# Optimization experiments

Measured on AMD Instinct MI355X. Metric: run time of the kernel, lower is better.

The kernel has to match this reference:

```python
import jax, jax.numpy as jnp
import numpy as np

B, N, NF, DEG = 128, 1024, 64, 16
NH = 128          # top-level n_hidden
H = NH // 2       # per-branch hidden (64)
NNODES = B * N
NEDGES = NNODES * DEG
ANG = 2


def _lin(key, fi, fo):
    k1, k2 = jax.random.split(key)
    s = 1.0 / np.sqrt(fi)
    return (jax.random.uniform(k1, (fi, fo), minval=-s, maxval=s, dtype=jnp.float32),
            jax.random.uniform(k2, (fo,), minval=-s, maxval=s, dtype=jnp.float32))

_PARAM_DEFS = [("W_pre1_a", "b_pre1_a", NF, H), ("W_pre2_a", "b_pre2_a", H, H), ("W_gcn_a", "b_gcn_a", H, H),
               ("W_pre1_b", "b_pre1_b", NF, H), ("W_pre2_b", "b_pre2_b", H, H), ("W_gcn_b", "b_gcn_b", H, H),
               ("W_lin1", "b_lin1", 2 * NH + 1, NH), ("W_lin2", "b_lin2", NH, NH // 2),
               ("W_lin3", "b_lin3", NH // 2, 1), ("W_cb", "b_cb", NH // 2, 1),
               ("W_om", "b_om", NH // 2, ANG), ("W_th", "b_th", NH // 2, ANG), ("W_ph", "b_ph", NH // 2, ANG)]


def setup_inputs() -> dict:
    key = jax.random.key(0)
    ks = jax.random.split(key, 24)

    def edges(k):
        # block-structured edges: each graph g owns nodes [g*N, (g+1)*N)
        e = jax.random.randint(k, (2, NEDGES), 0, N, dtype=jnp.int32)
        off = (jnp.arange(NEDGES, dtype=jnp.int32) // (N * DEG)) * N
        return e + off[None, :]

    batch = jnp.arange(NNODES, dtype=jnp.int32) // N
    inp = {
        "x_a": jax.random.normal(ks[0], (NNODES, NF), dtype=jnp.float32),
        "edge_index_a": edges(ks[1]),
        "edge_attr_a": jax.random.uniform(ks[2], (NEDGES,), dtype=jnp.float32),
        "x_a_batch": batch,
        "x_b": jax.random.normal(ks[3], (NNODES, NF), dtype=jnp.float32),
        "edge_index_b": edges(ks[4]),
        "edge_attr_b": jax.random.uniform(ks[5], (NEDGES,), dtype=jnp.float32),
        "x_b_batch": batch,
        "linker_size": jax.random.uniform(ks[6], (B, 1), dtype=jnp.float32),
    }
    for i, (wn, bn, fi, fo) in enumerate(_PARAM_DEFS):
        w, b = _lin(ks[7 + i], fi, fo)
        inp[wn] = w
        inp[bn] = b
    return inp


def _gcn(x, W, b, src, dst, ew, n):
    # GCNConv with edge weights and self loops (fill_value=1):
    #   out = D^{-1/2} (A + I) D^{-1/2} (x W) + b
    h = x @ W
    deg = jax.ops.segment_sum(ew, dst, num_segments=n) + 1.0
    dinv = jax.lax.rsqrt(deg)
    norm = dinv[src] * ew * dinv[dst]                        # [E]
    out = jax.ops.segment_sum(h[src] * norm[:, None], dst, num_segments=n)
    out = out + h * (dinv * dinv)[:, None]                   # self-loop contribution
    return out + b


def _branch(x, ei, ea, bat, Wp1, bp1, Wp2, bp2, Wg, bg):
    x = jax.nn.relu(x @ Wp1 + bp1)
    x = jax.nn.relu(x @ Wp2 + bp2)
    x = jax.nn.relu(_gcn(x, Wg, bg, ei[0], ei[1], ea, x.shape[0]))
    s = jax.ops.segment_sum(x, bat, num_segments=B)          # gsp: global sum pool
    cnt = jax.ops.segment_sum(jnp.ones((x.shape[0], 1), x.dtype), bat, num_segments=B)
    return jnp.concatenate([s, s / cnt], axis=1)             # [B, 2H] = [gsp || gap(mean)]


def reference(x_a, edge_index_a, edge_attr_a, x_a_batch,
              x_b, edge_index_b, edge_attr_b, x_b_batch, linker_size,
              W_pre1_a, b_pre1_a, W_pre2_a, b_pre2_a, W_gcn_a, b_gcn_a,
              W_pre1_b, b_pre1_b, W_pre2_b, b_pre2_b, W_gcn_b, b_gcn_b,
              W_lin1, b_lin1, W_lin2, b_lin2, W_lin3, b_lin3,
              W_cb, b_cb, W_om, b_om, W_th, b_th, W_ph, b_ph):
    xa = _branch(x_a, edge_index_a, edge_attr_a, x_a_batch,
                 W_pre1_a, b_pre1_a, W_pre2_a, b_pre2_a, W_gcn_a, b_gcn_a)
    xb = _branch(x_b, edge_index_b, edge_attr_b, x_b_batch,
                 W_pre1_b, b_pre1_b, W_pre2_b, b_pre2_b, W_gcn_b, b_gcn_b)
    x = jnp.concatenate([xa, xb, linker_size], axis=1)       # [B, 2*NH+1]
    x = jax.nn.relu(x @ W_lin1 + b_lin1)                     # dropout p=0.0 -> identity
    x = jax.nn.relu(x @ W_lin2 + b_lin2)
    ca = x @ W_lin3 + b_lin3                                 # loss_type='bce' -> no sigmoid
    cb = x @ W_cb + b_cb
    om = x @ W_om + b_om
    th = x @ W_th + b_th
    ph = x @ W_ph + b_ph
    return (ca, cb, om, th, ph)
```

## Files before the change

kernel.cpp:

```cpp
#include <hip/hip_runtime.h>
#include <hip/hip_bf16.h>

#define NNODES 131072
#define NEDGES 2097152
#define NB     128
#define NPG    1024
#define EPG    16384

#define OFF_DEG      0
#define OFF_POOLED   (OFF_DEG + 2*NNODES)
#define OFF_WT       (OFF_POOLED + 2*NB*64)
#define OFF_H        (OFF_WT + 6*4096)
#define OFF_CNT      (OFF_H + (size_t)2*NNODES*64)
#define OFF_ROWSTART (OFF_CNT + 2*NNODES)
#define OFF_CURSOR   (OFF_ROWSTART + 2*NNODES)
#define OFF_CSR      (OFF_CURSOR + 2*NNODES)
#define WS_NEEDED    ((OFF_CSR + (size_t)4*NEDGES) * 4)

#define CSRB_LDS 145408

typedef __attribute__((ext_vector_type(8))) short bfrag;
typedef __attribute__((ext_vector_type(4))) float f32x4;

__device__ __forceinline__ unsigned short f2bf(float v) {
    unsigned int u = __float_as_uint(v);
    unsigned int r = (u + 0x7fffu + ((u >> 16) & 1u)) >> 16;
    return (unsigned short)r;
}
__device__ __forceinline__ float bf2f(unsigned short s) {
    return __uint_as_float(((unsigned int)s) << 16);
}

__global__ void wprep(const float* __restrict__ w0, const float* __restrict__ w1,
                      const float* __restrict__ w2, const float* __restrict__ w3,
                      const float* __restrict__ w4, const float* __restrict__ w5,
                      unsigned short* __restrict__ wf) {
    int m = blockIdx.x;
    const float* w = (m == 0) ? w0 : (m == 1) ? w1 : (m == 2) ? w2
                   : (m == 3) ? w3 : (m == 4) ? w4 : w5;
    for (int idx = threadIdx.x; idx < 4096; idx += blockDim.x) {
        int ft   = idx >> 10;
        int kt   = (idx >> 9) & 1;
        int lane = (idx >> 3) & 63;
        int i    = idx & 7;
        int f = ft * 16 + (lane & 15);
        int k = kt * 32 + ((lane >> 4) << 3) + i;
        float v = w[k * 64 + f];
        unsigned short hi = f2bf(v);
        unsigned short lo = f2bf(v - bf2f(hi));
        wf[m * 8192 + idx]        = hi;
        wf[m * 8192 + 4096 + idx] = lo;
    }
}

__global__ __launch_bounds__(512) void csr_build2(
    const int* __restrict__ eia, const float* __restrict__ eaa,
    const int* __restrict__ eib, const float* __restrict__ eab,
    float* __restrict__ deg, int* __restrict__ rowstart,
    int* __restrict__ cnt, float2* __restrict__ csr) {
    extern __shared__ char smem[];
    float2* scsr = (float2*)smem;
    float*  sdeg = (float*)(smem + 131072);
    int*    scnt = (int*)(smem + 135168);
    int*    scur = (int*)(smem + 139264);
    int*    sm   = (int*)(smem + 143360);
    const int g  = blockIdx.x;
    const int br = blockIdx.y;
    const int* ei   = br ? eib : eia;
    const float* ea = br ? eab : eaa;
    const int t     = threadIdx.x;
    const int ebase = g * EPG;
    const int nbase = g * NPG;

    for (int i = t; i < NPG; i += 512) { sdeg[i] = 0.f; scnt[i] = 0; }
    __syncthreads();

#pragma unroll 4
    for (int it = 0; it < EPG / 512; ++it) {
        int e = ebase + it * 512 + t;
        int d = ei[NEDGES + e] - nbase;
        float w = ea[e];
        atomicAdd(&scnt[d], 1);
        atomicAdd(&sdeg[d], w);
    }
    __syncthreads();

    for (int i = t; i < NPG; i += 512) {
        float dv = sdeg[i];
        deg[br * NNODES + nbase + i] = dv;
        sdeg[i] = rsqrtf(dv + 1.f);
    }

    int c0 = scnt[t * 2 + 0], c1 = scnt[t * 2 + 1];
    int T = c0 + c1;
    sm[t] = T;
    __syncthreads();
    for (int off = 1; off < 512; off <<= 1) {
        int v = (t >= off) ? sm[t - off] : 0;
        __syncthreads();
        sm[t] += v;
        __syncthreads();
    }
    int excl = sm[t] - T;
    int r0 = excl, r1 = excl + c0;
    int nout = br * NNODES + nbase + t * 2;
    rowstart[nout + 0] = ebase + r0;
    rowstart[nout + 1] = ebase + r1;
    cnt[nout + 0] = c0; cnt[nout + 1] = c1;
    scur[t * 2 + 0] = r0; scur[t * 2 + 1] = r1;
    __syncthreads();

#pragma unroll 4
    for (int it = 0; it < EPG / 512; ++it) {
        int e = ebase + it * 512 + t;
        int srcg = ei[e];
        int s = srcg - nbase;
        int d = ei[NEDGES + e] - nbase;
        float w = ea[e];
        int pos = atomicAdd(&scur[d], 1);
        float2 pr;
        pr.x = __int_as_float(srcg);
        pr.y = sdeg[s] * w * sdeg[d];
        scsr[pos] = pr;
    }
    __syncthreads();

    float4* dst4 = (float4*)(csr + (size_t)br * NEDGES + ebase);
    const float4* src4 = (const float4*)scsr;
    for (int i = t; i < 8192; i += 512) dst4[i] = src4[i];
}

__global__ __launch_bounds__(256) void csr_build(
    const int* __restrict__ eia, const float* __restrict__ eaa,
    const int* __restrict__ eib, const float* __restrict__ eab,
    float* __restrict__ deg, int* __restrict__ rowstart,
    int* __restrict__ cnt, float2* __restrict__ csr) {
    __shared__ float sdeg[NPG];
    __shared__ int   scnt[NPG];
    __shared__ int   scur[NPG];
    __shared__ int   sm[256];
    const int g  = blockIdx.x;
    const int br = blockIdx.y;
    const int* ei   = br ? eib : eia;
    const float* ea = br ? eab : eaa;
    const int t     = threadIdx.x;
    const int ebase = g * EPG;
    const int nbase = g * NPG;

    for (int i = t; i < NPG; i += 256) { sdeg[i] = 0.f; scnt[i] = 0; }
    __syncthreads();
#pragma unroll 4
    for (int it = 0; it < EPG / 256; ++it) {
        int e = ebase + it * 256 + t;
        int d = ei[NEDGES + e] - nbase;
        float w = ea[e];
        atomicAdd(&scnt[d], 1);
        atomicAdd(&sdeg[d], w);
    }
    __syncthreads();
    for (int i = t; i < NPG; i += 256) {
        float dv = sdeg[i];
        deg[br * NNODES + nbase + i] = dv;
        sdeg[i] = rsqrtf(dv + 1.f);
    }
    int c0 = scnt[t * 4 + 0], c1 = scnt[t * 4 + 1], c2 = scnt[t * 4 + 2], c3 = scnt[t * 4 + 3];
    int T = c0 + c1 + c2 + c3;
    sm[t] = T;
    __syncthreads();
    for (int off = 1; off < 256; off <<= 1) {
        int v = (t >= off) ? sm[t - off] : 0;
        __syncthreads();
        sm[t] += v;
        __syncthreads();
    }
    int excl = sm[t] - T;
    int base = ebase + excl;
    int r0 = base, r1 = base + c0, r2 = r1 + c1, r3 = r2 + c2;
    int nout = br * NNODES + nbase + t * 4;
    rowstart[nout + 0] = r0; rowstart[nout + 1] = r1;
    rowstart[nout + 2] = r2; rowstart[nout + 3] = r3;
    cnt[nout + 0] = c0; cnt[nout + 1] = c1; cnt[nout + 2] = c2; cnt[nout + 3] = c3;
    scur[t * 4 + 0] = r0; scur[t * 4 + 1] = r1;
    scur[t * 4 + 2] = r2; scur[t * 4 + 3] = r3;
    __syncthreads();
    float2* cso = csr + (size_t)br * NEDGES;
#pragma unroll 4
    for (int it = 0; it < EPG / 256; ++it) {
        int e = ebase + it * 256 + t;
        int srcg = ei[e];
        int s = srcg - nbase;
        int d = ei[NEDGES + e] - nbase;
        float w = ea[e];
        int pos = atomicAdd(&scur[d], 1);
        float2 pr;
        pr.x = __int_as_float(srcg);
        pr.y = sdeg[s] * w * sdeg[d];
        cso[pos] = pr;
    }
}

__global__ __launch_bounds__(256) void node_mlp_mfma(
    const float* __restrict__ xa, const float* __restrict__ xb,
    const unsigned short* __restrict__ wf,
    const float* __restrict__ b1a, const float* __restrict__ b2a,
    const float* __restrict__ b1b, const float* __restrict__ b2b,
    float* __restrict__ hout) {
    __shared__ float lds[4 * 16 * 65];
    const int br = blockIdx.y;
    const float* x = br ? xb : xa;
    const unsigned short* wfb = wf + br * 3 * 8192;
    const float* b1 = br ? b1b : b1a;
    const float* b2 = br ? b2b : b2a;
    const int wave = threadIdx.x >> 6;
    const int lane = threadIdx.x & 63;
    const int row  = lane & 15;
    const int kg   = lane >> 4;
    const int n0   = blockIdx.x * 64 + wave * 16;
    float* wlds = &lds[wave * 16 * 65];

    bfrag ahi[2], alo[2];
#pragma unroll
    for (int kt = 0; kt < 2; ++kt) {
        const float4* p = reinterpret_cast<const float4*>(
            x + (size_t)(n0 + row) * 64 + kt * 32 + kg * 8);
        float4 v0 = p[0], v1 = p[1];
        float vv[8] = {v0.x, v0.y, v0.z, v0.w, v1.x, v1.y, v1.z, v1.w};
        bfrag h, l;
#pragma unroll
        for (int i = 0; i < 8; ++i) {
            unsigned short hb = f2bf(vv[i]);
            unsigned short lb = f2bf(vv[i] - bf2f(hb));
            h[i] = (short)hb;
            l[i] = (short)lb;
        }
        ahi[kt] = h; alo[kt] = l;
    }

#pragma unroll
    for (int layer = 0; layer < 3; ++layer) {
        const unsigned short* wl = wfb + layer * 8192;
        bfrag bhi[4][2], blo[4][2];
#pragma unroll
        for (int ft = 0; ft < 4; ++ft)
#pragma unroll
            for (int kt = 0; kt < 2; ++kt) {
                bhi[ft][kt] = *reinterpret_cast<const bfrag*>(wl + ft * 1024 + kt * 512 + lane * 8);
                blo[ft][kt] = *reinterpret_cast<const bfrag*>(wl + 4096 + ft * 1024 + kt * 512 + lane * 8);
            }
        f32x4 acc[4];
#pragma unroll
        for (int ft = 0; ft < 4; ++ft) {
            float bv = (layer == 0) ? b1[ft * 16 + row]
                     : (layer == 1) ? b2[ft * 16 + row] : 0.f;
            acc[ft] = (f32x4){bv, bv, bv, bv};
        }
#pragma unroll
        for (int ft = 0; ft < 4; ++ft)
#pragma unroll
            for (int kt = 0; kt < 2; ++kt) {
                acc[ft] = __builtin_amdgcn_mfma_f32_16x16x32_bf16(ahi[kt], bhi[ft][kt], acc[ft], 0, 0, 0);
                acc[ft] = __builtin_amdgcn_mfma_f32_16x16x32_bf16(alo[kt], bhi[ft][kt], acc[ft], 0, 0, 0);
                acc[ft] = __builtin_amdgcn_mfma_f32_16x16x32_bf16(ahi[kt], blo[ft][kt], acc[ft], 0, 0, 0);
            }

        if (layer < 2) {
#pragma unroll
            for (int ft = 0; ft < 4; ++ft)
#pragma unroll
                for (int r = 0; r < 4; ++r)
                    wlds[(kg * 4 + r) * 65 + ft * 16 + row] = fmaxf(acc[ft][r], 0.f);
            __syncthreads();
#pragma unroll
            for (int kt = 0; kt < 2; ++kt) {
                const float* rp = &wlds[row * 65 + kt * 32 + kg * 8];
                bfrag h, l;
#pragma unroll
                for (int i = 0; i < 8; ++i) {
                    float v = rp[i];
                    unsigned short hb = f2bf(v);
                    unsigned short lb = f2bf(v - bf2f(hb));
                    h[i] = (short)hb;
                    l[i] = (short)lb;
                }
                ahi[kt] = h; alo[kt] = l;
            }
            __syncthreads();
        } else {
            float* hp = hout + (size_t)br * NNODES * 64 + (size_t)n0 * 64;
#pragma unroll
            for (int ft = 0; ft < 4; ++ft)
#pragma unroll
                for (int r = 0; r < 4; ++r)
                    hp[(kg * 4 + r) * 64 + ft * 16 + row] = acc[ft][r];
        }
    }
}

__global__ __launch_bounds__(256) void gcn_gather_pool(
    const int* __restrict__ rowstart, const int* __restrict__ cnt,
    const float2* __restrict__ csr, const float* __restrict__ deg,
    const float* __restrict__ h,
    const float* __restrict__ bga, const float* __restrict__ bgb,
    float* __restrict__ pooled) {
    __shared__ float red[256];
    const int bid  = blockIdx.x;
    const int xcd  = bid & 7;
    const int sub  = bid >> 3;
    const int gb   = xcd * 32 + (sub >> 4);
    const int blk  = sub & 15;
    const int br   = gb >> 7;
    const int g    = gb & 127;
    const int wave = threadIdx.x >> 6;
    const int lane = threadIdx.x & 63;
    const int n0   = g * NPG + blk * 64 + wave * 16;

    const int*    rs = rowstart + br * NNODES;
    const int*    ct = cnt + br * NNODES;
    const float2* cs = csr + (size_t)br * NEDGES;
    const float*  dg = deg + br * NNODES;
    const float*  hh = h + (size_t)br * NNODES * 64;
    const float bias = (br ? bgb : bga)[lane];

    float psum = 0.f;
    for (int j = 0; j < 16; ++j) {
        int n = n0 + j;
        int r = __builtin_amdgcn_readfirstlane(rs[n]);
        int c = __builtin_amdgcn_readfirstlane(ct[n]);
        float a0 = 0.f, a1 = 0.f, a2 = 0.f, a3 = 0.f;
        int i = 0;
        for (; i + 4 <= c; i += 4) {
            float2 p0 = cs[r + i + 0];
            float2 p1 = cs[r + i + 1];
            float2 p2 = cs[r + i + 2];
            float2 p3 = cs[r + i + 3];
            a0 = fmaf(p0.y, hh[(size_t)__float_as_int(p0.x) * 64 + lane], a0);
            a1 = fmaf(p1.y, hh[(size_t)__float_as_int(p1.x) * 64 + lane], a1);
            a2 = fmaf(p2.y, hh[(size_t)__float_as_int(p2.x) * 64 + lane], a2);
            a3 = fmaf(p3.y, hh[(size_t)__float_as_int(p3.x) * 64 + lane], a3);
        }
        for (; i < c; ++i) {
            float2 p = cs[r + i];
            a0 = fmaf(p.y, hh[(size_t)__float_as_int(p.x) * 64 + lane], a0);
        }
        float d = dg[n] + 1.f;
        float v = (a0 + a1) + (a2 + a3) + hh[(size_t)n * 64 + lane] * (1.f / d) + bias;
        psum += fmaxf(v, 0.f);
    }
    red[threadIdx.x] = psum;
    __syncthreads();
    if (wave == 0) {
        float s = red[lane] + red[64 + lane] + red[128 + lane] + red[192 + lane];
        unsafeAtomicAdd(&pooled[br * (NB * 64) + g * 64 + lane], s);
    }
}

__global__ __launch_bounds__(128) void final_mlp(
    const float* __restrict__ pooled, const float* __restrict__ linker,
    const float* __restrict__ W1, const float* __restrict__ b1,
    const float* __restrict__ W2, const float* __restrict__ b2,
    const float* __restrict__ W3, const float* __restrict__ b3,
    const float* __restrict__ Wcb, const float* __restrict__ bcb,
    const float* __restrict__ Wom, const float* __restrict__ bom,
    const float* __restrict__ Wth, const float* __restrict__ bth,
    const float* __restrict__ Wph, const float* __restrict__ bph,
    float* __restrict__ out) {
    __shared__ float inv[260];
    __shared__ float x1[128];
    __shared__ float x2[64];
    const int g = blockIdx.x;
    const int t = threadIdx.x;
    if (t < 64) {
        float pa = pooled[g * 64 + t];
        float pb = pooled[NB * 64 + g * 64 + t];
        inv[t]       = pa;
        inv[64 + t]  = pa * (1.f / 1024.f);
        inv[128 + t] = pb;
        inv[192 + t] = pb * (1.f / 1024.f);
    }
    if (t == 0) inv[256] = linker[g];
    __syncthreads();

    {
        float a = b1[t];
        for (int i = 0; i < 257; ++i) a = fmaf(inv[i], W1[i * 128 + t], a);
        x1[t] = fmaxf(a, 0.f);
    }
    __syncthreads();
    if (t < 64) {
        float a = b2[t];
        for (int i = 0; i < 128; ++i) a = fmaf(x1[i], W2[i * 64 + t], a);
        x2[t] = fmaxf(a, 0.f);
    }
    __syncthreads();
    if (t < 8) {
        if (t == 0) {
            float a = b3[0];
            for (int i = 0; i < 64; ++i) a = fmaf(x2[i], W3[i], a);
            out[g] = a;
        } else if (t == 1) {
            float a = bcb[0];
            for (int i = 0; i < 64; ++i) a = fmaf(x2[i], Wcb[i], a);
            out[128 + g] = a;
        } else if (t < 4) {
            int j = t - 2; float a = bom[j];
            for (int i = 0; i < 64; ++i) a = fmaf(x2[i], Wom[i * 2 + j], a);
            out[256 + g * 2 + j] = a;
        } else if (t < 6) {
            int j = t - 4; float a = bth[j];
            for (int i = 0; i < 64; ++i) a = fmaf(x2[i], Wth[i * 2 + j], a);
            out[512 + g * 2 + j] = a;
        } else {
            int j = t - 6; float a = bph[j];
            for (int i = 0; i < 64; ++i) a = fmaf(x2[i], Wph[i * 2 + j], a);
            out[768 + g * 2 + j] = a;
        }
    }
}

extern "C" void kernel_launch(void* const* d_in, const int* in_sizes, int n_in,
                              void* d_out, int out_size, void* d_ws, size_t ws_size,
                              hipStream_t stream) {
    const float* x_a  = (const float*)d_in[0];
    const int*   ei_a = (const int*)d_in[1];
    const float* ea_a = (const float*)d_in[2];
    const float* x_b  = (const float*)d_in[4];
    const int*   ei_b = (const int*)d_in[5];
    const float* ea_b = (const float*)d_in[6];
    const float* linker = (const float*)d_in[8];
    const float* W_pre1_a = (const float*)d_in[9];
    const float* b_pre1_a = (const float*)d_in[10];
    const float* W_pre2_a = (const float*)d_in[11];
    const float* b_pre2_a = (const float*)d_in[12];
    const float* W_gcn_a  = (const float*)d_in[13];
    const float* b_gcn_a  = (const float*)d_in[14];
    const float* W_pre1_b = (const float*)d_in[15];
    const float* b_pre1_b = (const float*)d_in[16];
    const float* W_pre2_b = (const float*)d_in[17];
    const float* b_pre2_b = (const float*)d_in[18];
    const float* W_gcn_b  = (const float*)d_in[19];
    const float* b_gcn_b  = (const float*)d_in[20];
    const float* W_lin1 = (const float*)d_in[21];
    const float* b_lin1 = (const float*)d_in[22];
    const float* W_lin2 = (const float*)d_in[23];
    const float* b_lin2 = (const float*)d_in[24];
    const float* W_lin3 = (const float*)d_in[25];
    const float* b_lin3 = (const float*)d_in[26];
    const float* W_cb = (const float*)d_in[27];
    const float* b_cb = (const float*)d_in[28];
    const float* W_om = (const float*)d_in[29];
    const float* b_om = (const float*)d_in[30];
    const float* W_th = (const float*)d_in[31];
    const float* b_th = (const float*)d_in[32];
    const float* W_ph = (const float*)d_in[33];
    const float* b_ph = (const float*)d_in[34];

    float* ws     = (float*)d_ws;
    float* deg    = ws + OFF_DEG;
    float* pooled = ws + OFF_POOLED;
    float* wtw    = ws + OFF_WT;
    float* h      = ws + OFF_H;
    int*   cnt      = (int*)(ws + OFF_CNT);
    int*   rowstart = (int*)(ws + OFF_ROWSTART);
    float2* csr     = (float2*)(ws + OFF_CSR);

    hipMemsetAsync(pooled, 0, 2 * NB * 64 * sizeof(float), stream);
    wprep<<<6, 256, 0, stream>>>(W_pre1_a, W_pre2_a, W_gcn_a,
                                 W_pre1_b, W_pre2_b, W_gcn_b,
                                 (unsigned short*)wtw);

    hipError_t attr_ok = hipFuncSetAttribute(
        reinterpret_cast<const void*>(&csr_build2),
        hipFuncAttributeMaxDynamicSharedMemorySize, CSRB_LDS);
    if (attr_ok == hipSuccess) {
        csr_build2<<<dim3(NB, 2), 512, CSRB_LDS, stream>>>(ei_a, ea_a, ei_b, ea_b,
                                                           deg, rowstart, cnt, csr);
    } else {
        csr_build<<<dim3(NB, 2), 256, 0, stream>>>(ei_a, ea_a, ei_b, ea_b,
                                                   deg, rowstart, cnt, csr);
    }

    node_mlp_mfma<<<dim3(NNODES / 64, 2), 256, 0, stream>>>(
        x_a, x_b, (const unsigned short*)wtw,
        b_pre1_a, b_pre2_a, b_pre1_b, b_pre2_b, h);
    gcn_gather_pool<<<4096, 256, 0, stream>>>(rowstart, cnt, csr, deg, h,
                                              b_gcn_a, b_gcn_b, pooled);

    final_mlp<<<NB, 128, 0, stream>>>(pooled, linker,
                                      W_lin1, b_lin1, W_lin2, b_lin2, W_lin3, b_lin3,
                                      W_cb, b_cb, W_om, b_om, W_th, b_th, W_ph, b_ph,
                                      (float*)d_out);
}
```

Baseline: 405.8 us.

## Store node features in bf16, unroll gather by 8, nontemporal CSR loads

The node MLP output h is now written as bf16 instead of fp32, which halves the bytes the GCN gather has to pull for each neighbor. The gather loop is unrolled to 8 independent accumulators so more loads are in flight at once. CSR entries are read with nontemporal loads to limit cache pollution. The cost is reduced precision in h, which may move results closer to the tolerance limits.

```diff
diff --git a/kernel.cpp b/kernel.cpp
--- a/kernel.cpp
+++ b/kernel.cpp
@@ -29,6 +29,14 @@
 }
 __device__ __forceinline__ float bf2f(unsigned short s) {
     return __uint_as_float(((unsigned int)s) << 16);
+}
+__device__ __forceinline__ float2 ntload2(const float2* p) {
+    unsigned long long u = __builtin_nontemporal_load(
+        reinterpret_cast<const unsigned long long*>(p));
+    float2 r;
+    r.x = __uint_as_float((unsigned int)(u & 0xffffffffu));
+    r.y = __uint_as_float((unsigned int)(u >> 32));
+    return r;
 }
 
 __global__ void wprep(const float* __restrict__ w0, const float* __restrict__ w1,
@@ -204,7 +212,7 @@
     const unsigned short* __restrict__ wf,
     const float* __restrict__ b1a, const float* __restrict__ b2a,
     const float* __restrict__ b1b, const float* __restrict__ b2b,
-    float* __restrict__ hout) {
+    unsigned short* __restrict__ hout) {
     __shared__ float lds[4 * 16 * 65];
     const int br = blockIdx.y;
     const float* x = br ? xb : xa;
@@ -286,12 +294,12 @@
             }
             __syncthreads();
         } else {
-            float* hp = hout + (size_t)br * NNODES * 64 + (size_t)n0 * 64;
+            unsigned short* hp = hout + (size_t)br * NNODES * 64 + (size_t)n0 * 64;
 #pragma unroll
             for (int ft = 0; ft < 4; ++ft)
 #pragma unroll
                 for (int r = 0; r < 4; ++r)
-                    hp[(kg * 4 + r) * 64 + ft * 16 + row] = acc[ft][r];
+                    hp[(kg * 4 + r) * 64 + ft * 16 + row] = f2bf(acc[ft][r]);
         }
     }
 }
@@ -299,7 +307,7 @@
 __global__ __launch_bounds__(256) void gcn_gather_pool(
     const int* __restrict__ rowstart, const int* __restrict__ cnt,
     const float2* __restrict__ csr, const float* __restrict__ deg,
-    const float* __restrict__ h,
+    const unsigned short* __restrict__ h,
     const float* __restrict__ bga, const float* __restrict__ bgb,
     float* __restrict__ pooled) {
     __shared__ float red[256];
@@ -318,7 +326,7 @@
     const int*    ct = cnt + br * NNODES;
     const float2* cs = csr + (size_t)br * NEDGES;
     const float*  dg = deg + br * NNODES;
-    const float*  hh = h + (size_t)br * NNODES * 64;
+    const unsigned short* hh = h + (size_t)br * NNODES * 64;
     const float bias = (br ? bgb : bga)[lane];
 
     float psum = 0.f;
@@ -326,24 +334,44 @@
         int n = n0 + j;
         int r = __builtin_amdgcn_readfirstlane(rs[n]);
         int c = __builtin_amdgcn_readfirstlane(ct[n]);
-        float a0 = 0.f, a1 = 0.f, a2 = 0.f, a3 = 0.f;
+        float s0 = 0.f, s1 = 0.f, s2 = 0.f, s3 = 0.f;
+        float s4 = 0.f, s5 = 0.f, s6 = 0.f, s7 = 0.f;
         int i = 0;
+        for (; i + 8 <= c; i += 8) {
+            float2 p0 = ntload2(cs + r + i + 0);
+            float2 p1 = ntload2(cs + r + i + 1);
+            float2 p2 = ntload2(cs + r + i + 2);
+            float2 p3 = ntload2(cs + r + i + 3);
+            float2 p4 = ntload2(cs + r + i + 4);
+            float2 p5 = ntload2(cs + r + i + 5);
+            float2 p6 = ntload2(cs + r + i + 6);
+            float2 p7 = ntload2(cs + r + i + 7);
+            s0 = fmaf(p0.y, bf2f(hh[(size_t)__float_as_int(p0.x) * 64 + lane]), s0);
+            s1 = fmaf(p1.y, bf2f(hh[(size_t)__float_as_int(p1.x) * 64 + lane]), s1);
+            s2 = fmaf(p2.y, bf2f(hh[(size_t)__float_as_int(p2.x) * 64 + lane]), s2);
+            s3 = fmaf(p3.y, bf2f(hh[(size_t)__float_as_int(p3.x) * 64 + lane]), s3);
+            s4 = fmaf(p4.y, bf2f(hh[(size_t)__float_as_int(p4.x) * 64 + lane]), s4);
+            s5 = fmaf(p5.y, bf2f(hh[(size_t)__float_as_int(p5.x) * 64 + lane]), s5);
+            s6 = fmaf(p6.y, bf2f(hh[(size_t)__float_as_int(p6.x) * 64 + lane]), s6);
+            s7 = fmaf(p7.y, bf2f(hh[(size_t)__float_as_int(p7.x) * 64 + lane]), s7);
+        }
         for (; i + 4 <= c; i += 4) {
-            float2 p0 = cs[r + i + 0];
-            float2 p1 = cs[r + i + 1];
-            float2 p2 = cs[r + i + 2];
-            float2 p3 = cs[r + i + 3];
-            a0 = fmaf(p0.y, hh[(size_t)__float_as_int(p0.x) * 64 + lane], a0);
-            a1 = fmaf(p1.y, hh[(size_t)__float_as_int(p1.x) * 64 + lane], a1);
-            a2 = fmaf(p2.y, hh[(size_t)__float_as_int(p2.x) * 64 + lane], a2);
-            a3 = fmaf(p3.y, hh[(size_t)__float_as_int(p3.x) * 64 + lane], a3);
+            float2 p0 = ntload2(cs + r + i + 0);
+            float2 p1 = ntload2(cs + r + i + 1);
+            float2 p2 = ntload2(cs + r + i + 2);
+            float2 p3 = ntload2(cs + r + i + 3);
+            s0 = fmaf(p0.y, bf2f(hh[(size_t)__float_as_int(p0.x) * 64 + lane]), s0);
+            s1 = fmaf(p1.y, bf2f(hh[(size_t)__float_as_int(p1.x) * 64 + lane]), s1);
+            s2 = fmaf(p2.y, bf2f(hh[(size_t)__float_as_int(p2.x) * 64 + lane]), s2);
+            s3 = fmaf(p3.y, bf2f(hh[(size_t)__float_as_int(p3.x) * 64 + lane]), s3);
         }
         for (; i < c; ++i) {
-            float2 p = cs[r + i];
-            a0 = fmaf(p.y, hh[(size_t)__float_as_int(p.x) * 64 + lane], a0);
+            float2 p = ntload2(cs + r + i);
+            s0 = fmaf(p.y, bf2f(hh[(size_t)__float_as_int(p.x) * 64 + lane]), s0);
         }
         float d = dg[n] + 1.f;
-        float v = (a0 + a1) + (a2 + a3) + hh[(size_t)n * 64 + lane] * (1.f / d) + bias;
+        float v = ((s0 + s1) + (s2 + s3)) + ((s4 + s5) + (s6 + s7))
+                + bf2f(hh[(size_t)n * 64 + lane]) * (1.f / d) + bias;
         psum += fmaxf(v, 0.f);
     }
     red[threadIdx.x] = psum;
@@ -458,7 +486,7 @@
     float* deg    = ws + OFF_DEG;
     float* pooled = ws + OFF_POOLED;
     float* wtw    = ws + OFF_WT;
-    float* h      = ws + OFF_H;
+    unsigned short* h = (unsigned short*)(ws + OFF_H);
     int*   cnt      = (int*)(ws + OFF_CNT);
     int*   rowstart = (int*)(ws + OFF_ROWSTART);
     float2* csr     = (float2*)(ws + OFF_CSR);
```

Result: faster. 379.2 us (-6.6%).
